# Kernel optimization log

Measured on AMD Instinct MI355X. Metric: run time of the kernel, lower is better.

The kernel has to match this reference:

```python
import jax, jax.numpy as jnp
import numpy as np
from jax import lax

C = 512          # in_channels
L = 4            # fcos_conv_layers
NUM_CLS = 1      # fcos_num_class - 1
PRIOR_BIAS = float(-np.log((1 - 0.01) / 0.01))
BN_EPS = 1e-5


def conv1d(x, w, b, pad):
    # x: [B, Cin, T], w: [Cout, Cin, K]
    y = lax.conv_general_dilated(x, w, window_strides=(1,), padding=[(pad, pad)],
                                 dimension_numbers=('NCH', 'OIH', 'NCH'))
    return y + b[None, :, None]


def bn(x, g, b, m, v):
    inv = lax.rsqrt(v + BN_EPS)
    return (x - m[None, :, None]) * (g * inv)[None, :, None] + b[None, :, None]


def tower(x, ws, bs, gs, bes, ms, vs):
    # ws: [L, C, C, 3]; fixed small loop over layers
    for i in range(L):
        x = jax.nn.relu(bn(conv1d(x, ws[i], bs[i], 1), gs[i], bes[i], ms[i], vs[i]))
    return x


def setup_inputs() -> dict:
    key = jax.random.key(0)
    ks = jax.random.split(key, 32)
    d = {}
    d['f0'] = jax.random.normal(ks[0], (8, C, 1024), jnp.float32)
    d['f1'] = jax.random.normal(ks[1], (8, C, 512), jnp.float32)
    d['f2'] = jax.random.normal(ks[2], (8, C, 256), jnp.float32)

    def nrm(k, shape):
        return 0.01 * jax.random.normal(k, shape, jnp.float32)

    # cls / bbox towers: stacked conv + BN params
    d['cls_tw_w'] = nrm(ks[3], (L, C, C, 3)); d['cls_tw_b'] = jnp.zeros((L, C))
    d['cls_bn_g'] = jnp.ones((L, C)); d['cls_bn_b'] = jnp.zeros((L, C))
    d['cls_bn_m'] = jnp.zeros((L, C)); d['cls_bn_v'] = jnp.ones((L, C))
    d['box_tw_w'] = nrm(ks[4], (L, C, C, 3)); d['box_tw_b'] = jnp.zeros((L, C))
    d['box_bn_g'] = jnp.ones((L, C)); d['box_bn_b'] = jnp.zeros((L, C))
    d['box_bn_m'] = jnp.zeros((L, C)); d['box_bn_v'] = jnp.ones((L, C))

    d['logits_w'] = nrm(ks[5], (NUM_CLS, C, 3))
    d['logits_b'] = jnp.full((NUM_CLS,), PRIOR_BIAS, jnp.float32)
    d['bbox_w'] = nrm(ks[6], (2, C, 3)); d['bbox_b'] = jnp.zeros((2,))

    d['mix_w'] = nrm(ks[7], (C, 2 * C, 1)); d['mix_b'] = jnp.zeros((C,))
    d['mix_bn_g'] = jnp.ones((C,)); d['mix_bn_b'] = jnp.zeros((C,))
    d['mix_bn_m'] = jnp.zeros((C,)); d['mix_bn_v'] = jnp.ones((C,))

    d['iou_w1'] = nrm(ks[8], (C // 2, C, 3)); d['iou_b1'] = jnp.zeros((C // 2,))
    d['iou_bn_g'] = jnp.ones((C // 2,)); d['iou_bn_b'] = jnp.zeros((C // 2,))
    d['iou_bn_m'] = jnp.zeros((C // 2,)); d['iou_bn_v'] = jnp.ones((C // 2,))
    d['iou_w2'] = nrm(ks[9], (1, C // 2, 1)); d['iou_b2'] = jnp.zeros((1,))

    d['scales'] = jnp.ones((3,), jnp.float32)
    return d


def reference(f0, f1, f2,
              cls_tw_w, cls_tw_b, cls_bn_g, cls_bn_b, cls_bn_m, cls_bn_v,
              box_tw_w, box_tw_b, box_bn_g, box_bn_b, box_bn_m, box_bn_v,
              logits_w, logits_b, bbox_w, bbox_b,
              mix_w, mix_b, mix_bn_g, mix_bn_b, mix_bn_m, mix_bn_v,
              iou_w1, iou_b1, iou_bn_g, iou_bn_b, iou_bn_m, iou_bn_v,
              iou_w2, iou_b2, scales):
    outs = []
    for l, x in enumerate([f0, f1, f2]):
        ct = tower(x, cls_tw_w, cls_tw_b, cls_bn_g, cls_bn_b, cls_bn_m, cls_bn_v)
        bt = tower(x, box_tw_w, box_tw_b, box_bn_g, box_bn_b, box_bn_m, box_bn_v)
        logits = conv1d(ct, logits_w, logits_b, 1)                      # [B, 1, T]
        bbox = jnp.exp(conv1d(bt, bbox_w, bbox_b, 1) * scales[l])       # [B, 2, T]
        mix = jax.nn.relu(bn(conv1d(jnp.concatenate([ct, bt], axis=1), mix_w, mix_b, 0),
                             mix_bn_g, mix_bn_b, mix_bn_m, mix_bn_v))   # [B, C, T]
        h = jax.nn.relu(bn(conv1d(mix, iou_w1, iou_b1, 1),
                           iou_bn_g, iou_bn_b, iou_bn_m, iou_bn_v))
        iou = conv1d(h, iou_w2, iou_b2, 0)                              # [B, 1, T]
        outs.append(jnp.concatenate([logits, bbox, iou], axis=1))       # [B, 4, T]
    return jnp.concatenate(outs, axis=-1)  # [B, 4, T0+T1+T2]
```

## Files before the change

kernel.cpp:

```cpp
#include <hip/hip_runtime.h>
#include <hip/hip_bf16.h>


typedef __bf16 bf16x8 __attribute__((ext_vector_type(8)));
typedef float f32x4 __attribute__((ext_vector_type(4)));

__device__ __forceinline__ float bf2f(unsigned short u) {
    union { unsigned int i; float f; } c; c.i = ((unsigned int)u) << 16; return c.f;
}
__device__ __forceinline__ unsigned short f2bf(float f) {
    union { __hip_bfloat16 h; unsigned short u; } c; c.h = __float2bfloat16(f); return c.u;
}

__device__ __forceinline__ void gload16(const void* g, void* l) {
    __builtin_amdgcn_global_load_lds(
        (const __attribute__((address_space(1))) unsigned int*)g,
        (__attribute__((address_space(3))) unsigned int*)l,
        16, 0, 0);
}

__device__ __forceinline__ void tile_decode(int ct, int& rowstart, int& t0, int& Tl) {
    if (ct < 64)      { Tl = 1024; int b = ct >> 3;                 t0 = (ct & 7) << 7; rowstart = b * 1026 + 1; }
    else if (ct < 96) { Tl = 512;  int i = ct - 64; int b = i >> 2; t0 = (i & 3) << 7; rowstart = 8208 + b * 514 + 1; }
    else              { Tl = 256;  int i = ct - 96; int b = i >> 1; t0 = (i & 1) << 7; rowstart = 12320 + b * 258 + 1; }
}

__global__ __launch_bounds__(256, 2)
void conv_tower(const unsigned short* __restrict__ X, int xstride, int ci_twstride,
                const unsigned short* __restrict__ W,
                const float* __restrict__ Bs,
                unsigned short* __restrict__ Y)
{
    __shared__ alignas(16) unsigned short Xb[2][9 * 512];
    __shared__ alignas(16) unsigned short Wb[3][16 * 512];
    constexpr int XBSZ = 9 * 512;
    constexpr int WBSZ = 16 * 512;
    constexpr int XBYTES = XBSZ * 2;
    constexpr int WBYTES = WBSZ * 2;

    const int L = blockIdx.x;
    const int P = (L & 7) * 56 + (L >> 3);
    const int ct = P >> 2, sub = P & 3;
    const int tw = sub >> 1, co0 = (sub & 1) << 8;

    int rowstart, t0, Tl;
    tile_decode(ct, rowstart, t0, Tl);
    const int rtile = rowstart + t0;

    const int tid = threadIdx.x, lane = tid & 63, wid = tid >> 6;
    const int wco = (wid >> 1) << 7;
    const int wt  = (wid & 1) << 6;
    const int lr = lane & 15, sr = lane >> 4;

    const unsigned short* Wp = W + (size_t)tw * 3145728;
    const float* Bp = Bs + tw * 2048;
    const int co_out0 = tw * 512 + co0;
    const int ci_off = tw * ci_twstride;

    const unsigned short* xga[3]; unsigned short* xl[3];
#pragma unroll
    for (int p = 0; p < 3; ++p) {
        int seg = (p < 2) ? (p * 4 + wid) : 8;
        xl[p] = (unsigned short*)Xb[0] + seg * 512;
        int row = seg * 16 + (lane >> 2);
        int sc = (lane & 3) ^ ((row >> 1) & 3);
        xga[p] = X + (size_t)(rtile - 1 + row) * xstride + ci_off + sc * 8;
    }
    const unsigned short* wga[4]; unsigned short* wl[4];
#pragma unroll
    for (int p = 0; p < 4; ++p) {
        int seg = p * 4 + wid;
        wl[p] = (unsigned short*)Wb[0] + seg * 512;
        int row = seg * 16 + (lane >> 2);
        int sc = (lane & 3) ^ ((row >> 1) & 3);
        wga[p] = Wp + (size_t)(co0 + row) * 1536 + sc * 8;
    }

    int aoff[8];
#pragma unroll
    for (int mi = 0; mi < 8; ++mi) {
        int ra = wco + mi * 16 + lr;
        aoff[mi] = ra * 64 + (((sr ^ (ra >> 1)) & 3) << 4);
    }
    int boff[3][4];
#pragma unroll
    for (int kk = 0; kk < 3; ++kk)
#pragma unroll
        for (int ni = 0; ni < 4; ++ni) {
            int rb = wt + ni * 16 + lr + kk;
            boff[kk][ni] = rb * 64 + (((sr ^ (rb >> 1)) & 3) << 4);
        }

    f32x4 acc[8][4];
#pragma unroll
    for (int i = 0; i < 8; ++i)
#pragma unroll
        for (int j = 0; j < 4; ++j) acc[i][j] = (f32x4){0.f, 0.f, 0.f, 0.f};

#pragma unroll
    for (int p = 0; p < 3; ++p) gload16(xga[p], xl[p]);
#pragma unroll
    for (int p = 0; p < 4; ++p) {
        gload16(wga[p],       wl[p]);
        gload16(wga[p] + 512, wl[p] + WBSZ);
    }
    asm volatile("s_waitcnt vmcnt(0)" ::: "memory");
    __builtin_amdgcn_s_barrier();

#pragma unroll
    for (int s = 0; s < 48; ++s) {
        const int kk = s % 3, k0 = s / 3;
        if      (s == 47) asm volatile("s_waitcnt vmcnt(0)" ::: "memory");
        else if (s == 46) asm volatile("s_waitcnt vmcnt(4)" ::: "memory");
        else if (kk == 0) asm volatile("s_waitcnt vmcnt(4)" ::: "memory");
        else              asm volatile("s_waitcnt vmcnt(7)" ::: "memory");
        __builtin_amdgcn_s_barrier();

        if (s + 2 <= 47) {
            const int u = s + 2, ut = u % 3, uk = u / 3;
#pragma unroll
            for (int p = 0; p < 4; ++p)
                gload16(wga[p] + ut * 512 + uk * 32, wl[p] + ut * WBSZ);
        }
        if (kk == 0 && k0 + 1 <= 15) {
#pragma unroll
            for (int p = 0; p < 3; ++p)
                gload16(xga[p] + (k0 + 1) * 32, xl[p] + ((k0 + 1) & 1) * XBSZ);
        }

        const char* wbuf = (const char*)Wb[0] + (s % 3) * WBYTES;
        const char* xbuf = (const char*)Xb[0] + (k0 & 1) * XBYTES;
        bf16x8 af[8], bv[4];
#pragma unroll
        for (int mi = 0; mi < 8; ++mi)
            af[mi] = *(const bf16x8*)(wbuf + aoff[mi]);
#pragma unroll
        for (int ni = 0; ni < 4; ++ni)
            bv[ni] = *(const bf16x8*)(xbuf + boff[kk][ni]);
#pragma unroll
        for (int mi = 0; mi < 8; ++mi)
#pragma unroll
            for (int ni = 0; ni < 4; ++ni)
                acc[mi][ni] = __builtin_amdgcn_mfma_f32_16x16x32_bf16(af[mi], bv[ni], acc[mi][ni], 0, 0, 0);
        __builtin_amdgcn_s_barrier();
    }

    const int r4 = sr * 4;
#pragma unroll
    for (int mi = 0; mi < 8; ++mi) {
        int co_l = wco + mi * 16 + r4;
        float b0 = Bp[co0 + co_l + 0], b1 = Bp[co0 + co_l + 1];
        float b2 = Bp[co0 + co_l + 2], b3 = Bp[co0 + co_l + 3];
#pragma unroll
        for (int ni = 0; ni < 4; ++ni) {
            int t = wt + ni * 16 + lr;
            f32x4 a = acc[mi][ni];
            float v0 = fmaxf(a[0] + b0, 0.f), v1 = fmaxf(a[1] + b1, 0.f);
            float v2 = fmaxf(a[2] + b2, 0.f), v3 = fmaxf(a[3] + b3, 0.f);
            union { unsigned long long u; unsigned short s[4]; } pk2;
            pk2.s[0] = f2bf(v0); pk2.s[1] = f2bf(v1); pk2.s[2] = f2bf(v2); pk2.s[3] = f2bf(v3);
            *(unsigned long long*)(Y + (size_t)(rtile + t) * 1024 + co_out0 + co_l) = pk2.u;
        }
    }
}

template<int KSIZE>
__global__ __launch_bounds__(256)
void conv_gemm(const unsigned short* __restrict__ X, int xstride, int ci0_base, int ci_twstride, int Cin,
               const unsigned short* __restrict__ W, int w_twstride,
               const float* __restrict__ Bs, int b_twstride,
               unsigned short* __restrict__ Y, int ystride, int co_twstride,
               int relu)
{
    constexpr int BM = 128, BN = 128, BK = 32;
    constexpr int NR = BN + KSIZE - 1;
    constexpr int XSEG = (NR * 64 + 1023) / 1024;
    constexpr int XPW  = (XSEG + 3) / 4;
    constexpr int WSEG = KSIZE * BM * 64 / 1024;
    constexpr int WPW  = WSEG / 4;
    __shared__ alignas(16) unsigned short Xs[2 * XSEG * 512];
    __shared__ alignas(16) unsigned short Ws[2 * WSEG * 512];

    const int tid = threadIdx.x;
    const int lane = tid & 63, wid = tid >> 6;
    int rowstart, t0, Tl;
    tile_decode(blockIdx.x, rowstart, t0, Tl);
    const int co0 = blockIdx.y * BM;
    const int tw = blockIdx.z;
    const int ci_off = ci0_base + tw * ci_twstride;
    const unsigned short* Wp = W + (size_t)tw * w_twstride;
    const float* Bp = Bs + tw * b_twstride;
    const int co_out0 = tw * co_twstride + co0;

    const int wm = (wid >> 1) * 64, wn = (wid & 1) * 64;
    const int lr = lane & 15;
    const int sr = lane >> 4;

    const unsigned short* xga[XPW]; unsigned short* xl[XPW];
#pragma unroll
    for (int p = 0; p < XPW; ++p) {
        int seg = (KSIZE == 3) ? ((p < 2) ? p * 4 + wid : 8) : (p * 4 + wid);
        xl[p] = Xs + seg * 512;
        int g = seg * 64 + lane;
        int row = g >> 2, s = (g & 3) ^ ((row >> 1) & 3);
        xga[p] = X + (size_t)(rowstart + t0 - (KSIZE >> 1) + row) * xstride + ci_off + s * 8;
    }
    const unsigned short* wga[WPW]; unsigned short* wl[WPW];
#pragma unroll
    for (int p = 0; p < WPW; ++p) {
        int seg = p * 4 + wid;
        wl[p] = Ws + seg * 512;
        int g = seg * 64 + lane;
        int row = g >> 2, s = (g & 3) ^ ((row >> 1) & 3);
        int co = row & (BM - 1), kk = row >> 7;
        wga[p] = Wp + (size_t)(co0 + co) * (KSIZE * Cin) + kk * Cin + s * 8;
    }

    f32x4 acc[4][4];
#pragma unroll
    for (int i = 0; i < 4; ++i)
#pragma unroll
        for (int j = 0; j < 4; ++j) acc[i][j] = (f32x4){0.f, 0.f, 0.f, 0.f};

    auto STAGE = [&](int buf) {
#pragma unroll
        for (int p = 0; p < XPW; ++p) { gload16(xga[p], xl[p] + buf * (XSEG * 512)); xga[p] += BK; }
#pragma unroll
        for (int p = 0; p < WPW; ++p) { gload16(wga[p], wl[p] + buf * (WSEG * 512)); wga[p] += BK; }
    };

    const int nk = Cin / BK;
    STAGE(0);
    int cur = 0;
    for (int ks = 0; ks < nk; ++ks) {
        if (ks + 1 < nk) {
            STAGE(cur ^ 1);
            if constexpr (KSIZE == 3) asm volatile("s_waitcnt vmcnt(9)" ::: "memory");
            else                      asm volatile("s_waitcnt vmcnt(4)" ::: "memory");
        } else {
            asm volatile("s_waitcnt vmcnt(0)" ::: "memory");
        }
        __builtin_amdgcn_sched_barrier(0);
        __builtin_amdgcn_s_barrier();

        const char* bXs = (const char*)Xs + cur * (XSEG * 1024);
        const char* bWs = (const char*)Ws + cur * (WSEG * 1024);
#pragma unroll
        for (int kk = 0; kk < KSIZE; ++kk) {
            bf16x8 af[4], bv[4];
#pragma unroll
            for (int mi = 0; mi < 4; ++mi) {
                int ra = kk * BM + wm + mi * 16 + lr;
                af[mi] = *(const bf16x8*)(bWs + ra * 64 + (((sr ^ (ra >> 1)) & 3) << 4));
                int rb = wn + mi * 16 + lr + kk;
                bv[mi] = *(const bf16x8*)(bXs + rb * 64 + (((sr ^ (rb >> 1)) & 3) << 4));
            }
#pragma unroll
            for (int mi = 0; mi < 4; ++mi)
#pragma unroll
                for (int ni = 0; ni < 4; ++ni)
                    acc[mi][ni] = __builtin_amdgcn_mfma_f32_16x16x32_bf16(af[mi], bv[ni], acc[mi][ni], 0, 0, 0);
        }
        __builtin_amdgcn_sched_barrier(0);
        __builtin_amdgcn_s_barrier();
        cur ^= 1;
    }

    const int r4 = (lane >> 4) * 4;
#pragma unroll
    for (int mi = 0; mi < 4; ++mi) {
        int co_l = wm + mi * 16 + r4;
        float b0 = Bp[co0 + co_l + 0], b1 = Bp[co0 + co_l + 1];
        float b2 = Bp[co0 + co_l + 2], b3 = Bp[co0 + co_l + 3];
#pragma unroll
        for (int ni = 0; ni < 4; ++ni) {
            int t = t0 + wn + ni * 16 + lr;
            f32x4 a = acc[mi][ni];
            float v0 = a[0] + b0, v1 = a[1] + b1, v2 = a[2] + b2, v3 = a[3] + b3;
            if (relu) {
                v0 = fmaxf(v0, 0.f); v1 = fmaxf(v1, 0.f);
                v2 = fmaxf(v2, 0.f); v3 = fmaxf(v3, 0.f);
            }
            union { unsigned long long u; unsigned short s[4]; } pk;
            pk.s[0] = f2bf(v0); pk.s[1] = f2bf(v1); pk.s[2] = f2bf(v2); pk.s[3] = f2bf(v3);
            *(unsigned long long*)(Y + (size_t)(rowstart + t) * ystride + co_out0 + co_l) = pk.u;
        }
    }
}

__global__ __launch_bounds__(256)
void zero_pads(unsigned short* __restrict__ act0, unsigned short* __restrict__ catA,
               unsigned short* __restrict__ catB, unsigned short* __restrict__ mixo,
               unsigned short* __restrict__ iouh)
{
    int c = blockIdx.x >> 1, side = blockIdx.x & 1;
    int start, Tl;
    if (c < 8)       { start = c * 1026;               Tl = 1024; }
    else if (c < 16) { start = 8208 + (c - 8) * 514;   Tl = 512;  }
    else             { start = 12320 + (c - 16) * 258; Tl = 256;  }
    size_t prow = start + (side ? Tl + 1 : 0);
    int tid = threadIdx.x;
    uint4 z = make_uint4(0u, 0u, 0u, 0u);
    if (tid < 64)  *(uint4*)(act0 + prow * 512 + tid * 8) = z;
    if (tid < 128) { *(uint4*)(catA + prow * 1024 + tid * 8) = z;
                     *(uint4*)(catB + prow * 1024 + tid * 8) = z; }
    if (tid >= 128 && tid < 192) *(uint4*)(mixo + prow * 512 + (tid - 128) * 8) = z;
    if (tid >= 192 && tid < 224) *(uint4*)(iouh + prow * 256 + (tid - 192) * 8) = z;
}

__global__ __launch_bounds__(256)
void transpose_in(const float* __restrict__ f0, const float* __restrict__ f1, const float* __restrict__ f2,
                  unsigned short* __restrict__ act0)
{
    __shared__ float tile[32][33];
    int bx = blockIdx.x;
    const float* src; int Tl, padbase, b, t0;
    if (bx < 256)      { src = f0; Tl = 1024; int i = bx;       b = i >> 5; t0 = (i & 31) << 5; padbase = b * 1026; }
    else if (bx < 384) { src = f1; Tl = 512;  int i = bx - 256; b = i >> 4; t0 = (i & 15) << 5; padbase = 8208 + b * 514; }
    else               { src = f2; Tl = 256;  int i = bx - 384; b = i >> 3; t0 = (i & 7)  << 5; padbase = 12320 + b * 258; }
    int c0 = blockIdx.y << 5;
    const float* sb = src + (size_t)b * 512 * Tl;
    int tl = threadIdx.x & 31, cl = threadIdx.x >> 5;
#pragma unroll
    for (int j = 0; j < 4; ++j) {
        int c = cl + j * 8;
        tile[c][tl] = sb[(size_t)(c0 + c) * Tl + t0 + tl];
    }
    __syncthreads();
    int cc = threadIdx.x & 31, tr0 = threadIdx.x >> 5;
    size_t base = (size_t)(padbase + 1 + t0) * 512 + c0;
#pragma unroll
    for (int j = 0; j < 4; ++j) {
        int tr = tr0 + j * 8;
        act0[base + (size_t)tr * 512 + cc] = f2bf(tile[cc][tr]);
    }
}

__global__ __launch_bounds__(256)
void prep_tower(const float* __restrict__ cls_w, const float* __restrict__ box_w,
                const float* __restrict__ cg, const float* __restrict__ cvv,
                const float* __restrict__ bg, const float* __restrict__ bvv,
                unsigned short* __restrict__ Wt)
{
    int idx = blockIdx.x * 256 + threadIdx.x;
    if (idx >= 2 * 4 * 512 * 3 * 512) return;
    int ci = idx & 511;
    int kk = (idx >> 9) % 3;
    int co = (idx / 1536) & 511;
    int l  = (idx / 786432) & 3;
    int tw = idx / 3145728;
    const float* w = tw ? box_w : cls_w;
    const float* g = tw ? bg : cg;
    const float* v = tw ? bvv : cvv;
    float s = g[l * 512 + co] * rsqrtf(v[l * 512 + co] + 1e-5f);
    float val = w[(((size_t)(l * 512 + co)) * 512 + ci) * 3 + kk] * s;
    Wt[idx] = f2bf(val);
}

__global__ __launch_bounds__(256)
void prep_misc(const float* mix_w, const float* mix_b, const float* mg, const float* mbeta, const float* mm, const float* mv,
               const float* iou_w1, const float* iou_b1, const float* ig, const float* ibeta, const float* im, const float* iv,
               const float* cls_b, const float* cg, const float* cbeta, const float* cm, const float* cv2,
               const float* box_b, const float* bg, const float* bbeta, const float* bm, const float* bv2,
               unsigned short* Wmix, unsigned short* Wiou, float* Bt, float* Bmix, float* Biou)
{
    int idx = blockIdx.x * 256 + threadIdx.x;
    if (idx < 524288) {
        int co = idx >> 10;
        float s = mg[co] * rsqrtf(mv[co] + 1e-5f);
        Wmix[idx] = f2bf(mix_w[idx] * s);
        return;
    }
    idx -= 524288;
    if (idx < 393216) {
        int ci = idx & 511, kk = (idx >> 9) % 3, co = idx / 1536;
        float s = ig[co] * rsqrtf(iv[co] + 1e-5f);
        Wiou[idx] = f2bf(iou_w1[((size_t)(co * 512 + ci)) * 3 + kk] * s);
        return;
    }
    idx -= 393216;
    if (idx < 4096) {
        int co = idx & 511, l = (idx >> 9) & 3, tw = idx >> 11;
        const float* g = tw ? bg : cg; const float* v = tw ? bv2 : cv2;
        const float* m = tw ? bm : cm; const float* be = tw ? bbeta : cbeta;
        const float* cb = tw ? box_b : cls_b;
        int o = l * 512 + co;
        float s = g[o] * rsqrtf(v[o] + 1e-5f);
        Bt[idx] = (cb[o] - m[o]) * s + be[o];
        return;
    }
    idx -= 4096;
    if (idx < 512) {
        float s = mg[idx] * rsqrtf(mv[idx] + 1e-5f);
        Bmix[idx] = (mix_b[idx] - mm[idx]) * s + mbeta[idx];
        return;
    }
    idx -= 512;
    if (idx < 256) {
        float s = ig[idx] * rsqrtf(iv[idx] + 1e-5f);
        Biou[idx] = (iou_b1[idx] - im[idx]) * s + ibeta[idx];
    }
}

__global__ __launch_bounds__(256)
void heads_kernel(const unsigned short* __restrict__ catb, const unsigned short* __restrict__ iouh,
                  const float* __restrict__ lw, const float* __restrict__ lb,
                  const float* __restrict__ bw, const float* __restrict__ bb,
                  const float* __restrict__ iw, const float* __restrict__ ib,
                  const float* __restrict__ scales, float* __restrict__ out)
{
    const int lane = threadIdx.x & 63;
    const int wid = threadIdx.x >> 6;

    float lwr[24], bwr0[24], bwr1[24], iwr[4];
    {
        const float4* p = (const float4*)(lw + lane * 24);
#pragma unroll
        for (int q = 0; q < 6; ++q) {
            float4 v = p[q];
            lwr[q * 4 + 0] = v.x; lwr[q * 4 + 1] = v.y; lwr[q * 4 + 2] = v.z; lwr[q * 4 + 3] = v.w;
        }
        p = (const float4*)(bw + lane * 24);
#pragma unroll
        for (int q = 0; q < 6; ++q) {
            float4 v = p[q];
            bwr0[q * 4 + 0] = v.x; bwr0[q * 4 + 1] = v.y; bwr0[q * 4 + 2] = v.z; bwr0[q * 4 + 3] = v.w;
        }
        p = (const float4*)(bw + 1536 + lane * 24);
#pragma unroll
        for (int q = 0; q < 6; ++q) {
            float4 v = p[q];
            bwr1[q * 4 + 0] = v.x; bwr1[q * 4 + 1] = v.y; bwr1[q * 4 + 2] = v.z; bwr1[q * 4 + 3] = v.w;
        }
        float4 v = *(const float4*)(iw + lane * 4);
        iwr[0] = v.x; iwr[1] = v.y; iwr[2] = v.z; iwr[3] = v.w;
    }
    const float lb0 = lb[0], bb0 = bb[0], bb1 = bb[1], ib0 = ib[0];
    const float s0 = scales[0], s1 = scales[1], s2 = scales[2];

    for (int r = blockIdx.x * 4 + wid; r < 14336; r += gridDim.x * 4) {
        int tlog, roff, tgoff, padbase; float sc;
        if (r < 8192)       { tlog = 10; roff = 0;     tgoff = 0;    sc = s0; }
        else if (r < 12288) { tlog = 9;  roff = 8192;  tgoff = 1024; sc = s1; }
        else                { tlog = 8;  roff = 12288; tgoff = 1536; sc = s2; }
        int i = r - roff;
        int Tl = 1 << tlog;
        int b = i >> tlog, t = i & (Tl - 1);
        if (r < 8192)       padbase = b * 1026;
        else if (r < 12288) padbase = 8208 + b * 514;
        else                padbase = 12320 + b * 258;
        int prow = padbase + 1 + t;

        float al = 0.f, a0 = 0.f, a1 = 0.f, ai = 0.f;
        const unsigned short* base = catb + (size_t)prow * 1024 + lane * 8;
#pragma unroll
        for (int kk = 0; kk < 3; ++kk) {
            union { uint4 u; unsigned short s[8]; } cv, bvv;
            cv.u = *(const uint4*)(base + (kk - 1) * 1024);
            bvv.u = *(const uint4*)(base + (kk - 1) * 1024 + 512);
#pragma unroll
            for (int j = 0; j < 8; ++j) {
                float xc = bf2f(cv.s[j]);
                float xb = bf2f(bvv.s[j]);
                al = fmaf(xc, lwr[j * 3 + kk], al);
                a0 = fmaf(xb, bwr0[j * 3 + kk], a0);
                a1 = fmaf(xb, bwr1[j * 3 + kk], a1);
            }
        }
        {
            union { uint2 u; unsigned short s[4]; } hv;
            hv.u = *(const uint2*)(iouh + (size_t)prow * 256 + lane * 4);
#pragma unroll
            for (int j = 0; j < 4; ++j) ai = fmaf(bf2f(hv.s[j]), iwr[j], ai);
        }
#pragma unroll
        for (int off = 32; off > 0; off >>= 1) {
            al += __shfl_xor(al, off);
            a0 += __shfl_xor(a0, off);
            a1 += __shfl_xor(a1, off);
            ai += __shfl_xor(ai, off);
        }
        if (lane == 0) {
            int tg = tgoff + t;
            out[((size_t)b * 4 + 0) * 1792 + tg] = al + lb0;
            out[((size_t)b * 4 + 1) * 1792 + tg] = expf((a0 + bb0) * sc);
            out[((size_t)b * 4 + 2) * 1792 + tg] = expf((a1 + bb1) * sc);
            out[((size_t)b * 4 + 3) * 1792 + tg] = ai + ib0;
        }
    }
}

extern "C" void kernel_launch(void* const* d_in, const int* in_sizes, int n_in,
                              void* d_out, int out_size, void* d_ws, size_t ws_size,
                              hipStream_t stream)
{
    const float* f0       = (const float*)d_in[0];
    const float* f1       = (const float*)d_in[1];
    const float* f2       = (const float*)d_in[2];
    const float* cls_tw_w = (const float*)d_in[3];
    const float* cls_tw_b = (const float*)d_in[4];
    const float* cls_bn_g = (const float*)d_in[5];
    const float* cls_bn_b = (const float*)d_in[6];
    const float* cls_bn_m = (const float*)d_in[7];
    const float* cls_bn_v = (const float*)d_in[8];
    const float* box_tw_w = (const float*)d_in[9];
    const float* box_tw_b = (const float*)d_in[10];
    const float* box_bn_g = (const float*)d_in[11];
    const float* box_bn_b = (const float*)d_in[12];
    const float* box_bn_m = (const float*)d_in[13];
    const float* box_bn_v = (const float*)d_in[14];
    const float* logits_w = (const float*)d_in[15];
    const float* logits_b = (const float*)d_in[16];
    const float* bbox_w   = (const float*)d_in[17];
    const float* bbox_b   = (const float*)d_in[18];
    const float* mix_w    = (const float*)d_in[19];
    const float* mix_b    = (const float*)d_in[20];
    const float* mix_bn_g = (const float*)d_in[21];
    const float* mix_bn_b = (const float*)d_in[22];
    const float* mix_bn_m = (const float*)d_in[23];
    const float* mix_bn_v = (const float*)d_in[24];
    const float* iou_w1   = (const float*)d_in[25];
    const float* iou_b1   = (const float*)d_in[26];
    const float* iou_bn_g = (const float*)d_in[27];
    const float* iou_bn_b = (const float*)d_in[28];
    const float* iou_bn_m = (const float*)d_in[29];
    const float* iou_bn_v = (const float*)d_in[30];
    const float* iou_w2   = (const float*)d_in[31];
    const float* iou_b2   = (const float*)d_in[32];
    const float* scales   = (const float*)d_in[33];

    unsigned char* ws = (unsigned char*)d_ws;
    unsigned short* Wt   = (unsigned short*)(ws + 0);
    unsigned short* Wmix = (unsigned short*)(ws + 12582912);
    unsigned short* Wiou = (unsigned short*)(ws + 13631488);
    float*          Bt   = (float*)(ws + 14417920);
    float*          Bmix = (float*)(ws + 14434304);
    float*          Biou = (float*)(ws + 14436352);
    unsigned short* act0 = (unsigned short*)(ws + 14437376);
    unsigned short* catA = (unsigned short*)(ws + 29182976);
    unsigned short* catB = (unsigned short*)(ws + 58674176);
    unsigned short* mixo = (unsigned short*)(ws + 88165376);
    unsigned short* iouh = (unsigned short*)(ws + 102910976);

    zero_pads<<<dim3(48), dim3(256), 0, stream>>>(act0, catA, catB, mixo, iouh);
    prep_tower<<<dim3(24576), dim3(256), 0, stream>>>(cls_tw_w, box_tw_w, cls_bn_g, cls_bn_v,
                                                      box_bn_g, box_bn_v, Wt);
    prep_misc<<<dim3(3603), dim3(256), 0, stream>>>(mix_w, mix_b, mix_bn_g, mix_bn_b, mix_bn_m, mix_bn_v,
                                                    iou_w1, iou_b1, iou_bn_g, iou_bn_b, iou_bn_m, iou_bn_v,
                                                    cls_tw_b, cls_bn_g, cls_bn_b, cls_bn_m, cls_bn_v,
                                                    box_tw_b, box_bn_g, box_bn_b, box_bn_m, box_bn_v,
                                                    Wmix, Wiou, Bt, Bmix, Biou);
    transpose_in<<<dim3(448, 16), dim3(256), 0, stream>>>(f0, f1, f2, act0);

    conv_tower<<<dim3(448), dim3(256), 0, stream>>>(act0, 512, 0,    Wt,            Bt,        catA);
    conv_tower<<<dim3(448), dim3(256), 0, stream>>>(catA, 1024, 512, Wt + 786432,  Bt + 512,  catB);
    conv_tower<<<dim3(448), dim3(256), 0, stream>>>(catB, 1024, 512, Wt + 1572864, Bt + 1024, catA);
    conv_tower<<<dim3(448), dim3(256), 0, stream>>>(catA, 1024, 512, Wt + 2359296, Bt + 1536, catB);
    conv_gemm<1><<<dim3(112, 4, 1), 256, 0, stream>>>(catB, 1024, 0, 0, 1024,
                                                      Wmix, 0, Bmix, 0, mixo, 512, 0, 1);
    conv_gemm<3><<<dim3(112, 2, 1), 256, 0, stream>>>(mixo, 512, 0, 0, 512,
                                                      Wiou, 0, Biou, 0, iouh, 256, 0, 1);
    heads_kernel<<<dim3(896), dim3(256), 0, stream>>>(catB, iouh, logits_w, logits_b,
                                                      bbox_w, bbox_b, iou_w2, iou_b2, scales,
                                                      (float*)d_out);
}
```

Before: 284.4 us.

## Load tower weights directly from global into registers in MFMA fragment layout

The tower weights are now pre-permuted so each lane reads its A-fragment straight from global memory with one 16-byte load. This removes the shared-memory weight triple buffer and its barriers. Each wave now owns 64 output channels across all 128 time steps instead of a 128x64 tile, so the shared X tile is reused across 8 N-fragments and synchronisation happens only once per K chunk. The risk is exposed global-load latency, since only one step of register prefetch is used, and weight reads are no longer shared across waves through LDS.

Result: slower. 304.2 us (+7.0%).

```diff
diff --git a/kernel.cpp b/kernel.cpp
--- a/kernel.cpp
+++ b/kernel.cpp
@@ -32,11 +32,7 @@
                 unsigned short* __restrict__ Y)
 {
     __shared__ alignas(16) unsigned short Xb[2][9 * 512];
-    __shared__ alignas(16) unsigned short Wb[3][16 * 512];
     constexpr int XBSZ = 9 * 512;
-    constexpr int WBSZ = 16 * 512;
-    constexpr int XBYTES = XBSZ * 2;
-    constexpr int WBYTES = WBSZ * 2;
 
     const int L = blockIdx.x;
     const int P = (L & 7) * 56 + (L >> 3);
@@ -48,8 +44,6 @@
     const int rtile = rowstart + t0;
 
     const int tid = threadIdx.x, lane = tid & 63, wid = tid >> 6;
-    const int wco = (wid >> 1) << 7;
-    const int wt  = (wid & 1) << 6;
     const int lr = lane & 15, sr = lane >> 4;
 
     const unsigned short* Wp = W + (size_t)tw * 3145728;
@@ -66,94 +60,72 @@
         int sc = (lane & 3) ^ ((row >> 1) & 3);
         xga[p] = X + (size_t)(rtile - 1 + row) * xstride + ci_off + sc * 8;
     }
-    const unsigned short* wga[4]; unsigned short* wl[4];
-#pragma unroll
-    for (int p = 0; p < 4; ++p) {
-        int seg = p * 4 + wid;
-        wl[p] = (unsigned short*)Wb[0] + seg * 512;
-        int row = seg * 16 + (lane >> 2);
-        int sc = (lane & 3) ^ ((row >> 1) & 3);
-        wga[p] = Wp + (size_t)(co0 + row) * 1536 + sc * 8;
-    }
-
-    int aoff[8];
-#pragma unroll
-    for (int mi = 0; mi < 8; ++mi) {
-        int ra = wco + mi * 16 + lr;
-        aoff[mi] = ra * 64 + (((sr ^ (ra >> 1)) & 3) << 4);
-    }
-    int boff[3][4];
+
+    const int chunk0 = (co0 >> 4) + wid * 4;
+    const unsigned short* afp[4];
+#pragma unroll
+    for (int mi = 0; mi < 4; ++mi)
+        afp[mi] = Wp + (size_t)(chunk0 + mi) * 24576 + lane * 8;
+
+    int boff[3][8];
 #pragma unroll
     for (int kk = 0; kk < 3; ++kk)
 #pragma unroll
-        for (int ni = 0; ni < 4; ++ni) {
-            int rb = wt + ni * 16 + lr + kk;
+        for (int ni = 0; ni < 8; ++ni) {
+            int rb = ni * 16 + lr + kk;
             boff[kk][ni] = rb * 64 + (((sr ^ (rb >> 1)) & 3) << 4);
         }
 
-    f32x4 acc[8][4];
-#pragma unroll
-    for (int i = 0; i < 8; ++i)
-#pragma unroll
-        for (int j = 0; j < 4; ++j) acc[i][j] = (f32x4){0.f, 0.f, 0.f, 0.f};
+    f32x4 acc[4][8];
+#pragma unroll
+    for (int i = 0; i < 4; ++i)
+#pragma unroll
+        for (int j = 0; j < 8; ++j) acc[i][j] = (f32x4){0.f, 0.f, 0.f, 0.f};
 
 #pragma unroll
     for (int p = 0; p < 3; ++p) gload16(xga[p], xl[p]);
-#pragma unroll
-    for (int p = 0; p < 4; ++p) {
-        gload16(wga[p],       wl[p]);
-        gload16(wga[p] + 512, wl[p] + WBSZ);
-    }
-    asm volatile("s_waitcnt vmcnt(0)" ::: "memory");
-    __builtin_amdgcn_s_barrier();
+    bf16x8 af[2][4];
+#pragma unroll
+    for (int mi = 0; mi < 4; ++mi) af[0][mi] = *(const bf16x8*)(afp[mi]);
+    __syncthreads();
 
 #pragma unroll
     for (int s = 0; s < 48; ++s) {
         const int kk = s % 3, k0 = s / 3;
-        if      (s == 47) asm volatile("s_waitcnt vmcnt(0)" ::: "memory");
-        else if (s == 46) asm volatile("s_waitcnt vmcnt(4)" ::: "memory");
-        else if (kk == 0) asm volatile("s_waitcnt vmcnt(4)" ::: "memory");
-        else              asm volatile("s_waitcnt vmcnt(7)" ::: "memory");
-        __builtin_amdgcn_s_barrier();
-
-        if (s + 2 <= 47) {
-            const int u = s + 2, ut = u % 3, uk = u / 3;
-#pragma unroll
-            for (int p = 0; p < 4; ++p)
-                gload16(wga[p] + ut * 512 + uk * 32, wl[p] + ut * WBSZ);
-        }
-        if (kk == 0 && k0 + 1 <= 15) {
-#pragma unroll
-            for (int p = 0; p < 3; ++p)
-                gload16(xga[p] + (k0 + 1) * 32, xl[p] + ((k0 + 1) & 1) * XBSZ);
-        }
-
-        const char* wbuf = (const char*)Wb[0] + (s % 3) * WBYTES;
-        const char* xbuf = (const char*)Xb[0] + (k0 & 1) * XBYTES;
-        bf16x8 af[8], bv[4];
-#pragma unroll
-        for (int mi = 0; mi < 8; ++mi)
-            af[mi] = *(const bf16x8*)(wbuf + aoff[mi]);
-#pragma unroll
-        for (int ni = 0; ni < 4; ++ni)
+        if (kk == 0) {
+            if (k0 > 0) __syncthreads();
+            if (k0 + 1 < 16) {
+#pragma unroll
+                for (int p = 0; p < 3; ++p)
+                    gload16(xga[p] + (k0 + 1) * 32, xl[p] + ((k0 + 1) & 1) * XBSZ);
+            }
+        }
+        if (s + 1 < 48) {
+#pragma unroll
+            for (int mi = 0; mi < 4; ++mi)
+                af[(s + 1) & 1][mi] = *(const bf16x8*)(afp[mi] + (s + 1) * 512);
+        }
+        const char* xbuf = (const char*)Xb[0] + (k0 & 1) * (XBSZ * 2);
+        bf16x8 bv[8];
+#pragma unroll
+        for (int ni = 0; ni < 8; ++ni)
             bv[ni] = *(const bf16x8*)(xbuf + boff[kk][ni]);
 #pragma unroll
-        for (int mi = 0; mi < 8; ++mi)
-#pragma unroll
-            for (int ni = 0; ni < 4; ++ni)
-                acc[mi][ni] = __builtin_amdgcn_mfma_f32_16x16x32_bf16(af[mi], bv[ni], acc[mi][ni], 0, 0, 0);
-        __builtin_amdgcn_s_barrier();
+        for (int mi = 0; mi < 4; ++mi)
+#pragma unroll
+            for (int ni = 0; ni < 8; ++ni)
+                acc[mi][ni] = __builtin_amdgcn_mfma_f32_16x16x32_bf16(af[s & 1][mi], bv[ni], acc[mi][ni], 0, 0, 0);
     }
 
     const int r4 = sr * 4;
 #pragma unroll
-    for (int mi = 0; mi < 8; ++mi) {
-        int co_l = wco + mi * 16 + r4;
+    for (int mi = 0; mi < 4; ++mi) {
+        int co_l = wid * 64 + mi * 16 + r4;
         float b0 = Bp[co0 + co_l + 0], b1 = Bp[co0 + co_l + 1];
         float b2 = Bp[co0 + co_l + 2], b3 = Bp[co0 + co_l + 3];
 #pragma unroll
-        for (int ni = 0; ni < 4; ++ni) {
-            int t = wt + ni * 16 + lr;
+        for (int ni = 0; ni < 8; ++ni) {
+            int t = ni * 16 + lr;
             f32x4 a = acc[mi][ni];
             float v0 = fmaxf(a[0] + b0, 0.f), v1 = fmaxf(a[1] + b1, 0.f);
             float v2 = fmaxf(a[2] + b2, 0.f), v3 = fmaxf(a[3] + b3, 0.f);
@@ -343,17 +315,23 @@
                 unsigned short* __restrict__ Wt)
 {
     int idx = blockIdx.x * 256 + threadIdx.x;
-    if (idx >= 2 * 4 * 512 * 3 * 512) return;
-    int ci = idx & 511;
-    int kk = (idx >> 9) % 3;
-    int co = (idx / 1536) & 511;
-    int l  = (idx / 786432) & 3;
-    int tw = idx / 3145728;
+    if (idx >= 6291456) return;
+    int j     = idx & 7;
+    int lane  = (idx >> 3) & 63;
+    int rest  = idx >> 9;
+    int s     = rest % 48;
+    int rest2 = rest / 48;
+    int chunk = rest2 & 31;
+    int l     = (rest2 >> 5) & 3;
+    int tw    = rest2 >> 7;
+    int co = chunk * 16 + (lane & 15);
+    int kk = s % 3, ks = s / 3;
+    int ci = ks * 32 + (lane >> 4) * 8 + j;
     const float* w = tw ? box_w : cls_w;
     const float* g = tw ? bg : cg;
     const float* v = tw ? bvv : cvv;
-    float s = g[l * 512 + co] * rsqrtf(v[l * 512 + co] + 1e-5f);
-    float val = w[(((size_t)(l * 512 + co)) * 512 + ci) * 3 + kk] * s;
+    float sc = g[l * 512 + co] * rsqrtf(v[l * 512 + co] + 1e-5f);
+    float val = w[(((size_t)(l * 512 + co)) * 512 + ci) * 3 + kk] * sc;
     Wt[idx] = f2bf(val);
 }
 
```
